# Kernel tuning notes

Measured on AMD Instinct MI355X. Metric: run time of the kernel, lower is better.

The kernel has to match this reference:

```python
import jax, jax.numpy as jnp
import numpy as np

DT = 0.1
B_SZ = 8192
T_HIST = 20
LEN_PRED = 30
FEAT = 32
N_LAYERS = 3
# state transition for constant-acceleration model (matches self.F in torch)
F_MAT = np.array([[1.0, DT, DT * DT / 2], [0.0, 1.0, DT], [0.0, 0.0, 1.0]], dtype=np.float32)


def setup_inputs() -> dict:
    key = jax.random.key(0)
    ks = jax.random.split(key, 16)
    # random-walk trajectories as history observations
    hist = jnp.cumsum(jax.random.normal(ks[0], (B_SZ, T_HIST, 2), jnp.float32) * 0.5, axis=1)
    k_lin = 1.0 / np.sqrt(FEAT)
    k_in = 1.0 / np.sqrt(24)

    def u(k, shape, scale):
        return jax.random.uniform(k, shape, jnp.float32, -scale, scale)

    return {
        "hist": hist,
        "max_accel_x": jnp.ones((1,), jnp.float32) * 10.0,
        "max_accel_y": jnp.ones((1,), jnp.float32) * 20.0,
        "velocity_std_x": jnp.ones((1,), jnp.float32) * 10.0,
        "acceleration_std_x": jnp.ones((1,), jnp.float32) * 10.0,
        "R_x_": jnp.array([0.0448], jnp.float32),
        "R_y_": jnp.array([0.001], jnp.float32),
        "G_x": jnp.array([0.0059, 0.2981, 0.0393], jnp.float32),
        "G_y": jnp.array([0.0059, 0.2981, 0.0393], jnp.float32) / 5.0,
        "Win_W": u(ks[1], (FEAT, 24), k_in),
        "Win_b": u(ks[2], (FEAT,), k_in),
        "enc_Wih": u(ks[3], (N_LAYERS, 4 * FEAT, FEAT), k_lin),
        "enc_Whh": u(ks[4], (N_LAYERS, 4 * FEAT, FEAT), k_lin),
        "enc_bih": u(ks[5], (N_LAYERS, 4 * FEAT), k_lin),
        "enc_bhh": u(ks[6], (N_LAYERS, 4 * FEAT), k_lin),
        "dec_Wih": u(ks[7], (N_LAYERS, 4 * FEAT, FEAT), k_lin),
        "dec_Whh": u(ks[8], (N_LAYERS, 4 * FEAT, FEAT), k_lin),
        "dec_bih": u(ks[9], (N_LAYERS, 4 * FEAT), k_lin),
        "dec_bhh": u(ks[10], (N_LAYERS, 4 * FEAT), k_lin),
        "Wout_W": u(ks[11], (4, FEAT), k_lin),
        "Wout_b": u(ks[12], (4,), k_lin),
        "len_pred": LEN_PRED,
    }


def reference(hist, max_accel_x, max_accel_y, velocity_std_x, acceleration_std_x,
              R_x_, R_y_, G_x, G_y, Win_W, Win_b,
              enc_Wih, enc_Whh, enc_bih, enc_bhh,
              dec_Wih, dec_Whh, dec_bih, dec_bhh,
              Wout_W, Wout_b, len_pred):
    B = hist.shape[0]
    F = jnp.asarray(F_MAT)
    R_x = R_x_[0] * R_x_[0]
    R_y = R_y_[0] * R_y_[0]
    Z_x = hist[:, :, 0]
    Z_y = hist[:, :, 1]

    def lstm(x, h, c, Wih, Whh, bih, bhh):
        g = x @ Wih.T + bih + h @ Whh.T + bhh
        i, f, gg, o = jnp.split(g, 4, axis=1)
        c = jax.nn.sigmoid(f) * c + jax.nn.sigmoid(i) * jnp.tanh(gg)
        h = jax.nn.sigmoid(o) * jnp.tanh(c)
        return h, c

    def stack(XP, h, c, Wih, Whh, bih, bhh):
        x = jnp.tanh(XP @ Win_W.T + Win_b)
        hs, cs = [], []
        for j in range(N_LAYERS):
            hj, cj = lstm(x, h[j], c[j], Wih[j], Whh[j], bih[j], bhh[j])
            hs.append(hj)
            cs.append(cj)
            x = cj  # torch code feeds the fresh CELL state to the next layer
        return jnp.stack(hs), jnp.stack(cs)

    def kpred(X, P, Q):
        return X @ F.T, jnp.einsum('ij,bjk,lk->bil', F, P, F) + Q

    def kupdate(X, P, z, R):
        y = z - X[:, 0]                      # innovation (H picks component 0)
        S = P[:, 0, 0] + R                   # innovation covariance (scalar)
        K = P[:, :, 0] / S[:, None]          # Kalman gain (B,3)
        return X + y[:, None] * K, P - K[:, :, None] * P[:, 0:1, :]

    def kinit(z0):
        # torch always calls _kalman_init with is_x=True (default), so both
        # axes use R_x / velocity_std_x / acceleration_std_x
        X = jnp.zeros((B, 3), hist.dtype).at[:, 0].set(z0)
        d = jnp.stack([R_x, velocity_std_x[0] ** 2, acceleration_std_x[0] ** 2])
        P = jnp.zeros((B, 3, 3), hist.dtype).at[:, jnp.arange(3), jnp.arange(3)].set(d)
        return X, P

    Qx_e = jnp.outer(G_x * max_accel_x[0], G_x * max_accel_x[0])
    Qy_e = jnp.outer(G_y * max_accel_y[0], G_y * max_accel_y[0])

    Xx, Px = kinit(Z_x[:, 0])
    Xy, Py = kinit(Z_y[:, 0])
    h = jnp.zeros((N_LAYERS, B, FEAT), hist.dtype)
    c = jnp.zeros_like(h)

    def enc_step(carry, zs):
        Xx, Px, Xy, Py, h, c = carry
        zx, zy = zs
        XP = jnp.concatenate([Xx, Xy, Px.reshape(B, 9), Py.reshape(B, 9)], 1)
        h, c = stack(XP, h, c, enc_Wih, enc_Whh, enc_bih, enc_bhh)
        Xx, Px = kpred(Xx, Px, Qx_e)
        Xy, Py = kpred(Xy, Py, Qy_e)
        Xx, Px = kupdate(Xx, Px, zx, R_x)
        Xy, Py = kupdate(Xy, Py, zy, R_y)
        return (Xx, Px, Xy, Py, h, c), None

    carry, _ = jax.lax.scan(enc_step, (Xx, Px, Xy, Py, h, c),
                            (Z_x[:, 1:].T, Z_y[:, 1:].T))

    oxx = jnp.outer(G_x, G_x)
    oyy = jnp.outer(G_y, G_y)

    def dec_step(carry, _):
        Xx, Px, Xy, Py, h, c = carry
        XP = jnp.concatenate([Xx, Xy, Px.reshape(B, 9), Py.reshape(B, 9)], 1)
        h, c = stack(XP, h, c, dec_Wih, dec_Whh, dec_bih, dec_bhh)
        pred = c[-1] @ Wout_W.T + Wout_b  # (B,4): [u_x, u_y, std_x, std_y]
        Xx = Xx.at[:, 2].set(DT * pred[:, 0])  # X[:,2] = B*u
        Xy = Xy.at[:, 2].set(DT * pred[:, 1])
        Qx = (pred[:, 2] ** 2)[:, None, None] * oxx
        Qy = (pred[:, 3] ** 2)[:, None, None] * oyy
        Xx, Px = kpred(Xx, Px, Qx)
        Xy, Py = kpred(Xy, Py, Qy)
        out = jnp.stack([Xx[:, 0], Xy[:, 0],
                         jnp.sqrt(Px[:, 0, 0]), jnp.sqrt(Py[:, 0, 0]),
                         jnp.zeros(B, hist.dtype)], axis=1)  # (B,5)
        return (Xx, Px, Xy, Py, h, c), out

    carry, ys = jax.lax.scan(dec_step, carry, None, length=len_pred)
    return jnp.transpose(ys, (1, 0, 2))  # (B, len_pred, 5)
```

## Files before the change

kernel.cpp:

```cpp
#include <hip/hip_runtime.h>
#include <math.h>

#define DT   0.1f
#define HDT  0.005f
#define T_HIST 20
#define LEN_PRED 30

typedef __attribute__((ext_vector_type(8))) short bfrag8;
typedef __attribute__((ext_vector_type(4))) short short4v;
typedef __attribute__((ext_vector_type(4))) float f32x4;

#define WS_FRAG   0u
#define WS_WIN    98304u
#define WS_WOUT   100352u
#define WS_BIAS   101376u

static __device__ __forceinline__ unsigned short f2bf(float x) {
    union { float f; unsigned int u; } v; v.f = x;
    unsigned int r = v.u + 0x7fffu + ((v.u >> 16) & 1u);
    return (unsigned short)(r >> 16);
}

__global__ void prep_kernel(const float* __restrict__ Win_W,
                            const float* __restrict__ eWih, const float* __restrict__ eWhh,
                            const float* __restrict__ ebih, const float* __restrict__ ebhh,
                            const float* __restrict__ dWih, const float* __restrict__ dWhh,
                            const float* __restrict__ dbih, const float* __restrict__ dbhh,
                            const float* __restrict__ Wout_W,
                            char* __restrict__ ws)
{
    int i = blockIdx.x * blockDim.x + threadIdx.x;
    if (i < 49152) {
        int fi = i >> 9, within = i & 511;
        int lane = within >> 3, jj = within & 7;
        int c = fi & 1, j = (fi >> 1) & 1, wvv = (fi >> 2) & 3;
        int pl = fi >> 4;
        int l = pl % 3, ph = pl / 3;
        int m = lane & 15, q2 = lane >> 4;
        int gate = m & 3;
        int feat = wvv * 8 + 4 * j + (m >> 2);
        int row = gate * 32 + feat;
        int k = q2 * 8 + jj;
        const float* W = (c == 0) ? (ph ? dWih : eWih) : (ph ? dWhh : eWhh);
        ((unsigned short*)(ws + WS_FRAG))[i] = f2bf(W[l * 4096 + row * 32 + k]);
    } else if (i < 50176) {
        int i2 = i - 49152;
        int w = i2 >> 9, within = i2 & 511;
        int lane = within >> 3, jj = within & 7;
        int m = lane & 15, q2 = lane >> 4;
        int k = q2 * 8 + jj;
        float v = (k < 24) ? Win_W[(w * 16 + m) * 24 + k] : 0.f;
        ((unsigned short*)(ws + WS_WIN))[i2] = f2bf(v);
    } else if (i < 50688) {
        int i3 = i - 50176;
        int lane = i3 >> 3, jj = i3 & 7;
        int m = lane & 15, q2 = lane >> 4;
        float v = (m < 4) ? Wout_W[m * 32 + q2 * 8 + jj] : 0.f;
        ((unsigned short*)(ws + WS_WOUT))[i3] = f2bf(v);
    } else if (i < 51456) {
        int b = i - 50688;
        int ph = b / 384, rem = b % 384;
        int l = rem >> 7, row = rem & 127;
        const float* bi = ph ? dbih : ebih;
        const float* bh = ph ? dbhh : ebhh;
        ((float*)(ws + WS_BIAS))[b] = bi[l * 128 + row] + bh[l * 128 + row];
    }
}

__launch_bounds__(256, 2)
__global__ void kalman_lstm_kernel(const float* __restrict__ hist,
                                   const float* __restrict__ max_ax, const float* __restrict__ max_ay,
                                   const float* __restrict__ vstd, const float* __restrict__ astd,
                                   const float* __restrict__ Rx_, const float* __restrict__ Ry_,
                                   const float* __restrict__ Gx, const float* __restrict__ Gy,
                                   const float* __restrict__ Win_b, const float* __restrict__ Wout_b,
                                   const char* __restrict__ ws, float* __restrict__ out)
{
    __shared__ __align__(16) unsigned short xin[4][16][40];
    __shared__ __align__(16) unsigned short hbuf[2][3][16][40];
    __shared__ __align__(16) unsigned short xpw[2][16][40];

    const int tid  = threadIdx.x;
    const int wv   = tid >> 6;
    const int lane = tid & 63;
    const int q    = lane >> 4;
    const int m    = lane & 15;
    const int b_elem = blockIdx.x * 16 + m;

    bfrag8 fragA[3][2][2];
    float  biasR[3][2][4];
    const bfrag8* fragp = (const bfrag8*)(ws + WS_FRAG);
    const float*  combp = (const float*)(ws + WS_BIAS);
    auto load_phase = [&](int ph) {
#pragma unroll
        for (int l = 0; l < 3; ++l)
#pragma unroll
            for (int j = 0; j < 2; ++j) {
#pragma unroll
                for (int c = 0; c < 2; ++c) {
                    int fi = (((ph * 3 + l) * 4 + wv) * 2 + j) * 2 + c;
                    fragA[l][j][c] = fragp[fi * 64 + lane];
                }
#pragma unroll
                for (int r = 0; r < 4; ++r)
                    biasR[l][j][r] = combp[ph * 384 + l * 128 + r * 32 + (wv * 8 + 4 * j + q)];
            }
    };
    load_phase(0);

    bfrag8 winF = {}, woutF = {};
    f32x4 winB = {0.f, 0.f, 0.f, 0.f};
    float wb0 = 0.f, wb1 = 0.f, wb2 = 0.f, wb3 = 0.f;
    float g0 = 0.f, g1 = 0.f, g2 = 0.f, ge0 = 0.f, ge1 = 0.f, ge2 = 0.f;
    float Rch = 0.f, X0 = 0.f, X1 = 0.f, X2 = 0.f;
    float P00 = 0.f, P01 = 0.f, P02 = 0.f, P11 = 0.f, P12 = 0.f, P22 = 0.f;
    const int ch = q & 1;
    if (wv >= 2) {
        int w = wv - 2;
        winF  = ((const bfrag8*)(ws + WS_WIN))[w * 64 + lane];
        woutF = ((const bfrag8*)(ws + WS_WOUT))[lane];
#pragma unroll
        for (int r = 0; r < 4; ++r) winB[r] = Win_b[w * 16 + q * 4 + r];
        wb0 = Wout_b[0]; wb1 = Wout_b[1]; wb2 = Wout_b[2]; wb3 = Wout_b[3];
        const float rx = Rx_[0] * Rx_[0], ry = Ry_[0] * Ry_[0];
        Rch = ch ? ry : rx;
        if (ch == 0) { g0 = Gx[0]; g1 = Gx[1]; g2 = Gx[2]; float s = max_ax[0]; ge0 = g0*s; ge1 = g1*s; ge2 = g2*s; }
        else         { g0 = Gy[0]; g1 = Gy[1]; g2 = Gy[2]; float s = max_ay[0]; ge0 = g0*s; ge1 = g1*s; ge2 = g2*s; }
        X0 = hist[b_elem * (T_HIST * 2) + ch];
        P00 = Rch; P11 = vstd[0] * vstd[0]; P22 = astd[0] * astd[0];
    }

    float creg[3][2];
#pragma unroll
    for (int l = 0; l < 3; ++l) { creg[l][0] = 0.f; creg[l][1] = 0.f; }

    for (int idx = tid; idx < 4 * 16 * 40; idx += 256) (&xin[0][0][0])[idx] = 0;
    for (int idx = tid; idx < 2 * 3 * 16 * 40; idx += 256) (&hbuf[0][0][0][0])[idx] = 0;
    for (int idx = tid; idx < 2 * 16 * 40; idx += 256) (&xpw[0][0][0])[idx] = 0;

    auto sig = [](float z) { return __builtin_amdgcn_rcpf(1.f + __expf(-z)); };
    auto th  = [](float z) { return fmaf(-2.f, __builtin_amdgcn_rcpf(__expf(2.f * z) + 1.f), 1.f); };

    auto kpred = [&](float Q00, float Q01, float Q02, float Q11, float Q12, float Q22) {
        X0 = X0 + DT * X1 + HDT * X2;
        X1 = X1 + DT * X2;
        float M00 = P00 + DT * P01 + HDT * P02;
        float M01 = P01 + DT * P11 + HDT * P12;
        float M02 = P02 + DT * P12 + HDT * P22;
        float M11 = P11 + DT * P12;
        float M12 = P12 + DT * P22;
        float M22 = P22;
        P00 = M00 + DT * M01 + HDT * M02 + Q00;
        P01 = M01 + DT * M02 + Q01;
        P02 = M02 + Q02;
        P11 = M11 + DT * M12 + Q11;
        P12 = M12 + Q12;
        P22 = M22 + Q22;
    };
    auto kupdate = [&](float z) {
        float y = z - X0;
        float Sinv = 1.0f / (P00 + Rch);
        float K0 = P00 * Sinv, K1 = P01 * Sinv, K2 = P02 * Sinv;
        X0 += y * K0; X1 += y * K1; X2 += y * K2;
        float p00 = P00, p01 = P01, p02 = P02;
        P00 = p00 - K0 * p00;
        P01 = p01 - K0 * p01;
        P02 = p02 - K0 * p02;
        P11 = P11 - K1 * p01;
        P12 = P12 - K1 * p02;
        P22 = P22 - K2 * p02;
    };
    auto write_xp = [&]() {
        if (q < 2) {
            unsigned short* row = &xpw[wv - 2][m][0];
            int o = ch * 3;
            row[o + 0] = f2bf(X0); row[o + 1] = f2bf(X1); row[o + 2] = f2bf(X2);
            int pb = 6 + ch * 9;
            row[pb + 0] = f2bf(P00); row[pb + 1] = f2bf(P01); row[pb + 2] = f2bf(P02);
            row[pb + 3] = f2bf(P01); row[pb + 4] = f2bf(P11); row[pb + 5] = f2bf(P12);
            row[pb + 6] = f2bf(P02); row[pb + 7] = f2bf(P12); row[pb + 8] = f2bf(P22);
        }
    };

    const f32x4 zero4 = {0.f, 0.f, 0.f, 0.f};

    auto regionA = [&](int mode, int t) {
        if (wv >= 2) {
            if (mode == 0) {
                if (t > 0) {
                    float z = hist[b_elem * (T_HIST * 2) + t * 2 + ch];
                    kpred(ge0 * ge0, ge0 * ge1, ge0 * ge2, ge1 * ge1, ge1 * ge2, ge2 * ge2);
                    kupdate(z);
                }
            } else {
                if (t == 0) {
                    float z = hist[b_elem * (T_HIST * 2) + 19 * 2 + ch];
                    kpred(ge0 * ge0, ge0 * ge1, ge0 * ge2, ge1 * ge1, ge1 * ge2, ge2 * ge2);
                    kupdate(z);
                } else {
                    bfrag8 bc2 = *(const bfrag8*)&xin[3][m][q * 8];
                    f32x4 ap = __builtin_amdgcn_mfma_f32_16x16x32_bf16(woutF, bc2, zero4, 0, 0, 0);
                    float a0 = ap[0] + wb0, a1 = ap[1] + wb1, a2 = ap[2] + wb2, a3 = ap[3] + wb3;
                    float s0 = __shfl(a0, m), s1 = __shfl(a1, m);
                    float s2 = __shfl(a2, m), s3 = __shfl(a3, m);
                    float pe = ch ? s1 : s0;
                    float qe = ch ? s3 : s2;
                    X2 = DT * pe;
                    float qs = qe * qe;
                    kpred(qs*g0*g0, qs*g0*g1, qs*g0*g2, qs*g1*g1, qs*g1*g2, qs*g2*g2);
                    if (wv == 2 && q < 2) {
                        float* o = out + (size_t)b_elem * (LEN_PRED * 5) + (t - 1) * 5;
                        if (ch == 0) { o[0] = X0; o[2] = sqrtf(P00); }
                        else         { o[1] = X0; o[3] = sqrtf(P00); o[4] = 0.f; }
                    }
                }
            }
            write_xp();
            bfrag8 bxp = *(const bfrag8*)&xpw[wv - 2][m][q * 8];
            f32x4 aw = __builtin_amdgcn_mfma_f32_16x16x32_bf16(winF, bxp, zero4, 0, 0, 0);
            union { short4v v; unsigned short s[4]; } u;
#pragma unroll
            for (int r = 0; r < 4; ++r) u.s[r] = f2bf(th(aw[r] + winB[r]));
            *(short4v*)&xin[0][m][(wv - 2) * 16 + q * 4] = u.v;
        }
        __syncthreads();
    };

    auto layers = [&](int p) {
#pragma unroll
        for (int l = 0; l < 3; ++l) {
            bfrag8 bx = *(const bfrag8*)&xin[l][m][q * 8];
            bfrag8 bh = *(const bfrag8*)&hbuf[p][l][m][q * 8];
            f32x4 a0 = __builtin_amdgcn_mfma_f32_16x16x32_bf16(fragA[l][0][0], bx, zero4, 0, 0, 0);
            a0        = __builtin_amdgcn_mfma_f32_16x16x32_bf16(fragA[l][0][1], bh, a0, 0, 0, 0);
            f32x4 a1 = __builtin_amdgcn_mfma_f32_16x16x32_bf16(fragA[l][1][0], bx, zero4, 0, 0, 0);
            a1        = __builtin_amdgcn_mfma_f32_16x16x32_bf16(fragA[l][1][1], bh, a1, 0, 0, 0);
#pragma unroll
            for (int j = 0; j < 2; ++j) {
                f32x4 a = j ? a1 : a0;
                float iv = sig(a[0] + biasR[l][j][0]);
                float fv = sig(a[1] + biasR[l][j][1]);
                float gv = th (a[2] + biasR[l][j][2]);
                float ov = sig(a[3] + biasR[l][j][3]);
                float cn = fmaf(fv, creg[l][j], iv * gv);
                float hn = ov * th(cn);
                creg[l][j] = cn;
                int f = wv * 8 + 4 * j + q;
                xin[l + 1][m][f] = f2bf(cn);
                hbuf[p ^ 1][l][m][f] = f2bf(hn);
            }
            __syncthreads();
        }
    };

    __syncthreads();
    int p = 0;

    for (int t = 0; t < T_HIST - 1; ++t) { regionA(0, t); layers(p); p ^= 1; }
    load_phase(1);
    for (int t = 0; t < LEN_PRED; ++t)   { regionA(1, t); layers(p); p ^= 1; }

    if (wv == 2) {
        bfrag8 bc2 = *(const bfrag8*)&xin[3][m][q * 8];
        f32x4 ap = __builtin_amdgcn_mfma_f32_16x16x32_bf16(woutF, bc2, zero4, 0, 0, 0);
        float a0 = ap[0] + wb0, a1 = ap[1] + wb1, a2 = ap[2] + wb2, a3 = ap[3] + wb3;
        float s0 = __shfl(a0, m), s1 = __shfl(a1, m);
        float s2 = __shfl(a2, m), s3 = __shfl(a3, m);
        float pe = ch ? s1 : s0;
        float qe = ch ? s3 : s2;
        X2 = DT * pe;
        float qs = qe * qe;
        kpred(qs*g0*g0, qs*g0*g1, qs*g0*g2, qs*g1*g1, qs*g1*g2, qs*g2*g2);
        if (q < 2) {
            float* o = out + (size_t)b_elem * (LEN_PRED * 5) + (LEN_PRED - 1) * 5;
            if (ch == 0) { o[0] = X0; o[2] = sqrtf(P00); }
            else         { o[1] = X0; o[3] = sqrtf(P00); o[4] = 0.f; }
        }
    }
}

extern "C" void kernel_launch(void* const* d_in, const int* in_sizes, int n_in,
                              void* d_out, int out_size, void* d_ws, size_t ws_size,
                              hipStream_t stream)
{
    const float* hist  = (const float*)d_in[0];
    const float* maxax = (const float*)d_in[1];
    const float* maxay = (const float*)d_in[2];
    const float* vstd  = (const float*)d_in[3];
    const float* astd  = (const float*)d_in[4];
    const float* Rx    = (const float*)d_in[5];
    const float* Ry    = (const float*)d_in[6];
    const float* Gx    = (const float*)d_in[7];
    const float* Gy    = (const float*)d_in[8];
    const float* WinW  = (const float*)d_in[9];
    const float* Winb  = (const float*)d_in[10];
    const float* eWih  = (const float*)d_in[11];
    const float* eWhh  = (const float*)d_in[12];
    const float* ebih  = (const float*)d_in[13];
    const float* ebhh  = (const float*)d_in[14];
    const float* dWih  = (const float*)d_in[15];
    const float* dWhh  = (const float*)d_in[16];
    const float* dbih  = (const float*)d_in[17];
    const float* dbhh  = (const float*)d_in[18];
    const float* WoutW = (const float*)d_in[19];
    const float* Woutb = (const float*)d_in[20];
    char* ws = (char*)d_ws;
    float* out = (float*)d_out;

    prep_kernel<<<202, 256, 0, stream>>>(WinW, eWih, eWhh, ebih, ebhh,
                                         dWih, dWhh, dbih, dbhh, WoutW, ws);
    kalman_lstm_kernel<<<512, 256, 0, stream>>>(hist, maxax, maxay, vstd, astd,
                                                Rx, Ry, Gx, Gy, Winb, Woutb,
                                                ws, out);
}
```

Measured before the change: 193.9 us.

## Split LSTM gate MFMA and activation across 8 waves, fold exp scaling into weights

The block grows from 256 to 512 threads. Waves 0-3 run the gate MFMAs and write the pre-activations to LDS, all 8 waves then apply the activations with one feature per lane, and waves 6-7 run the Kalman/input projection. The sigmoid and tanh scaling constants (-log2e, 2log2e) are folded into the weights and biases at prep time, so activations reduce to exp2 plus rcp. Biases are moved from registers into the MFMA accumulator init, loaded from LDS. This spreads the serial transcendental work across more lanes, at the cost of an extra LDS round trip and an extra barrier per layer.

After: 260.7 us. 34.5% more time.

```diff
diff --git a/kernel.cpp b/kernel.cpp
--- a/kernel.cpp
+++ b/kernel.cpp
@@ -5,6 +5,8 @@
 #define HDT  0.005f
 #define T_HIST 20
 #define LEN_PRED 30
+#define NLOG2E   (-1.4426950408889634f)
+#define TWOLOG2E ( 2.8853900817779268f)
 
 typedef __attribute__((ext_vector_type(8))) short bfrag8;
 typedef __attribute__((ext_vector_type(4))) short short4v;
@@ -19,6 +21,10 @@
     union { float f; unsigned int u; } v; v.f = x;
     unsigned int r = v.u + 0x7fffu + ((v.u >> 16) & 1u);
     return (unsigned short)(r >> 16);
+}
+
+static __device__ __forceinline__ float rcp1(float z) {
+    return __builtin_amdgcn_rcpf(1.f + __builtin_amdgcn_exp2f(z));
 }
 
 __global__ void prep_kernel(const float* __restrict__ Win_W,
@@ -41,15 +47,16 @@
         int feat = wvv * 8 + 4 * j + (m >> 2);
         int row = gate * 32 + feat;
         int k = q2 * 8 + jj;
+        float scale = (gate == 2) ? TWOLOG2E : NLOG2E;
         const float* W = (c == 0) ? (ph ? dWih : eWih) : (ph ? dWhh : eWhh);
-        ((unsigned short*)(ws + WS_FRAG))[i] = f2bf(W[l * 4096 + row * 32 + k]);
+        ((unsigned short*)(ws + WS_FRAG))[i] = f2bf(W[l * 4096 + row * 32 + k] * scale);
     } else if (i < 50176) {
         int i2 = i - 49152;
         int w = i2 >> 9, within = i2 & 511;
         int lane = within >> 3, jj = within & 7;
         int m = lane & 15, q2 = lane >> 4;
         int k = q2 * 8 + jj;
-        float v = (k < 24) ? Win_W[(w * 16 + m) * 24 + k] : 0.f;
+        float v = (k < 24) ? Win_W[(w * 16 + m) * 24 + k] * TWOLOG2E : 0.f;
         ((unsigned short*)(ws + WS_WIN))[i2] = f2bf(v);
     } else if (i < 50688) {
         int i3 = i - 50176;
@@ -60,14 +67,17 @@
     } else if (i < 51456) {
         int b = i - 50688;
         int ph = b / 384, rem = b % 384;
-        int l = rem >> 7, row = rem & 127;
+        int l = rem >> 7, fg = rem & 127;
+        int feat = fg >> 2, gate = fg & 3;
+        int row = gate * 32 + feat;
+        float scale = (gate == 2) ? TWOLOG2E : NLOG2E;
         const float* bi = ph ? dbih : ebih;
         const float* bh = ph ? dbhh : ebhh;
-        ((float*)(ws + WS_BIAS))[b] = bi[l * 128 + row] + bh[l * 128 + row];
+        ((float*)(ws + WS_BIAS))[b] = (bi[l * 128 + row] + bh[l * 128 + row]) * scale;
     }
 }
 
-__launch_bounds__(256, 2)
+__launch_bounds__(512, 2)
 __global__ void kalman_lstm_kernel(const float* __restrict__ hist,
                                    const float* __restrict__ max_ax, const float* __restrict__ max_ay,
                                    const float* __restrict__ vstd, const float* __restrict__ astd,
@@ -79,6 +89,8 @@
     __shared__ __align__(16) unsigned short xin[4][16][40];
     __shared__ __align__(16) unsigned short hbuf[2][3][16][40];
     __shared__ __align__(16) unsigned short xpw[2][16][40];
+    __shared__ __align__(16) float bias_lds[2][3][32][4];
+    __shared__ __align__(16) float pre[512][4];
 
     const int tid  = threadIdx.x;
     const int wv   = tid >> 6;
@@ -88,25 +100,19 @@
     const int b_elem = blockIdx.x * 16 + m;
 
     bfrag8 fragA[3][2][2];
-    float  biasR[3][2][4];
     const bfrag8* fragp = (const bfrag8*)(ws + WS_FRAG);
-    const float*  combp = (const float*)(ws + WS_BIAS);
     auto load_phase = [&](int ph) {
 #pragma unroll
         for (int l = 0; l < 3; ++l)
 #pragma unroll
-            for (int j = 0; j < 2; ++j) {
+            for (int j = 0; j < 2; ++j)
 #pragma unroll
                 for (int c = 0; c < 2; ++c) {
                     int fi = (((ph * 3 + l) * 4 + wv) * 2 + j) * 2 + c;
                     fragA[l][j][c] = fragp[fi * 64 + lane];
                 }
-#pragma unroll
-                for (int r = 0; r < 4; ++r)
-                    biasR[l][j][r] = combp[ph * 384 + l * 128 + r * 32 + (wv * 8 + 4 * j + q)];
-            }
-    };
-    load_phase(0);
+    };
+    if (wv < 4) load_phase(0);
 
     bfrag8 winF = {}, woutF = {};
     f32x4 winB = {0.f, 0.f, 0.f, 0.f};
@@ -115,12 +121,12 @@
     float Rch = 0.f, X0 = 0.f, X1 = 0.f, X2 = 0.f;
     float P00 = 0.f, P01 = 0.f, P02 = 0.f, P11 = 0.f, P12 = 0.f, P22 = 0.f;
     const int ch = q & 1;
-    if (wv >= 2) {
-        int w = wv - 2;
+    if (wv >= 6) {
+        int w = wv - 6;
         winF  = ((const bfrag8*)(ws + WS_WIN))[w * 64 + lane];
         woutF = ((const bfrag8*)(ws + WS_WOUT))[lane];
 #pragma unroll
-        for (int r = 0; r < 4; ++r) winB[r] = Win_b[w * 16 + q * 4 + r];
+        for (int r = 0; r < 4; ++r) winB[r] = Win_b[w * 16 + q * 4 + r] * TWOLOG2E;
         wb0 = Wout_b[0]; wb1 = Wout_b[1]; wb2 = Wout_b[2]; wb3 = Wout_b[3];
         const float rx = Rx_[0] * Rx_[0], ry = Ry_[0] * Ry_[0];
         Rch = ch ? ry : rx;
@@ -130,16 +136,13 @@
         P00 = Rch; P11 = vstd[0] * vstd[0]; P22 = astd[0] * astd[0];
     }
 
-    float creg[3][2];
-#pragma unroll
-    for (int l = 0; l < 3; ++l) { creg[l][0] = 0.f; creg[l][1] = 0.f; }
-
-    for (int idx = tid; idx < 4 * 16 * 40; idx += 256) (&xin[0][0][0])[idx] = 0;
-    for (int idx = tid; idx < 2 * 3 * 16 * 40; idx += 256) (&hbuf[0][0][0][0])[idx] = 0;
-    for (int idx = tid; idx < 2 * 16 * 40; idx += 256) (&xpw[0][0][0])[idx] = 0;
-
-    auto sig = [](float z) { return __builtin_amdgcn_rcpf(1.f + __expf(-z)); };
-    auto th  = [](float z) { return fmaf(-2.f, __builtin_amdgcn_rcpf(__expf(2.f * z) + 1.f), 1.f); };
+    float creg[3] = {0.f, 0.f, 0.f};
+
+    for (int idx = tid; idx < 768; idx += 512)
+        ((float*)bias_lds)[idx] = ((const float*)(ws + WS_BIAS))[idx];
+    for (int idx = tid; idx < 4 * 16 * 40; idx += 512) (&xin[0][0][0])[idx] = 0;
+    for (int idx = tid; idx < 2 * 3 * 16 * 40; idx += 512) (&hbuf[0][0][0][0])[idx] = 0;
+    for (int idx = tid; idx < 2 * 16 * 40; idx += 512) (&xpw[0][0][0])[idx] = 0;
 
     auto kpred = [&](float Q00, float Q01, float Q02, float Q11, float Q12, float Q22) {
         X0 = X0 + DT * X1 + HDT * X2;
@@ -170,9 +173,9 @@
         P12 = P12 - K1 * p02;
         P22 = P22 - K2 * p02;
     };
-    auto write_xp = [&]() {
+    auto write_xp = [&](int w) {
         if (q < 2) {
-            unsigned short* row = &xpw[wv - 2][m][0];
+            unsigned short* row = &xpw[w][m][0];
             int o = ch * 3;
             row[o + 0] = f2bf(X0); row[o + 1] = f2bf(X1); row[o + 2] = f2bf(X2);
             int pb = 6 + ch * 9;
@@ -185,7 +188,8 @@
     const f32x4 zero4 = {0.f, 0.f, 0.f, 0.f};
 
     auto regionA = [&](int mode, int t) {
-        if (wv >= 2) {
+        if (wv >= 6) {
+            int w = wv - 6;
             if (mode == 0) {
                 if (t > 0) {
                     float z = hist[b_elem * (T_HIST * 2) + t * 2 + ch];
@@ -208,59 +212,64 @@
                     X2 = DT * pe;
                     float qs = qe * qe;
                     kpred(qs*g0*g0, qs*g0*g1, qs*g0*g2, qs*g1*g1, qs*g1*g2, qs*g2*g2);
-                    if (wv == 2 && q < 2) {
+                    if (wv == 6 && q < 2) {
                         float* o = out + (size_t)b_elem * (LEN_PRED * 5) + (t - 1) * 5;
                         if (ch == 0) { o[0] = X0; o[2] = sqrtf(P00); }
                         else         { o[1] = X0; o[3] = sqrtf(P00); o[4] = 0.f; }
                     }
                 }
             }
-            write_xp();
-            bfrag8 bxp = *(const bfrag8*)&xpw[wv - 2][m][q * 8];
-            f32x4 aw = __builtin_amdgcn_mfma_f32_16x16x32_bf16(winF, bxp, zero4, 0, 0, 0);
+            write_xp(w);
+            bfrag8 bxp = *(const bfrag8*)&xpw[w][m][q * 8];
+            f32x4 aw = __builtin_amdgcn_mfma_f32_16x16x32_bf16(winF, bxp, winB, 0, 0, 0);
             union { short4v v; unsigned short s[4]; } u;
 #pragma unroll
-            for (int r = 0; r < 4; ++r) u.s[r] = f2bf(th(aw[r] + winB[r]));
-            *(short4v*)&xin[0][m][(wv - 2) * 16 + q * 4] = u.v;
+            for (int r = 0; r < 4; ++r) u.s[r] = f2bf(fmaf(-2.f, rcp1(aw[r]), 1.f));
+            *(short4v*)&xin[0][m][w * 16 + q * 4] = u.v;
         }
         __syncthreads();
     };
 
-    auto layers = [&](int p) {
+    auto layers = [&](int ph, int p) {
 #pragma unroll
         for (int l = 0; l < 3; ++l) {
-            bfrag8 bx = *(const bfrag8*)&xin[l][m][q * 8];
-            bfrag8 bh = *(const bfrag8*)&hbuf[p][l][m][q * 8];
-            f32x4 a0 = __builtin_amdgcn_mfma_f32_16x16x32_bf16(fragA[l][0][0], bx, zero4, 0, 0, 0);
-            a0        = __builtin_amdgcn_mfma_f32_16x16x32_bf16(fragA[l][0][1], bh, a0, 0, 0, 0);
-            f32x4 a1 = __builtin_amdgcn_mfma_f32_16x16x32_bf16(fragA[l][1][0], bx, zero4, 0, 0, 0);
-            a1        = __builtin_amdgcn_mfma_f32_16x16x32_bf16(fragA[l][1][1], bh, a1, 0, 0, 0);
-#pragma unroll
-            for (int j = 0; j < 2; ++j) {
-                f32x4 a = j ? a1 : a0;
-                float iv = sig(a[0] + biasR[l][j][0]);
-                float fv = sig(a[1] + biasR[l][j][1]);
-                float gv = th (a[2] + biasR[l][j][2]);
-                float ov = sig(a[3] + biasR[l][j][3]);
-                float cn = fmaf(fv, creg[l][j], iv * gv);
-                float hn = ov * th(cn);
-                creg[l][j] = cn;
-                int f = wv * 8 + 4 * j + q;
-                xin[l + 1][m][f] = f2bf(cn);
-                hbuf[p ^ 1][l][m][f] = f2bf(hn);
+            if (wv < 4) {
+                bfrag8 bx = *(const bfrag8*)&xin[l][m][q * 8];
+                bfrag8 bh = *(const bfrag8*)&hbuf[p][l][m][q * 8];
+                f32x4 b0 = *(const f32x4*)&bias_lds[ph][l][wv * 8 + q][0];
+                f32x4 b1 = *(const f32x4*)&bias_lds[ph][l][wv * 8 + 4 + q][0];
+                f32x4 t0 = __builtin_amdgcn_mfma_f32_16x16x32_bf16(fragA[l][0][0], bx, b0, 0, 0, 0);
+                f32x4 a0 = __builtin_amdgcn_mfma_f32_16x16x32_bf16(fragA[l][0][1], bh, t0, 0, 0, 0);
+                f32x4 t1 = __builtin_amdgcn_mfma_f32_16x16x32_bf16(fragA[l][1][0], bx, b1, 0, 0, 0);
+                f32x4 a1 = __builtin_amdgcn_mfma_f32_16x16x32_bf16(fragA[l][1][1], bh, t1, 0, 0, 0);
+                *(f32x4*)&pre[(wv * 8 + q) * 16 + m][0] = a0;
+                *(f32x4*)&pre[(wv * 8 + 4 + q) * 16 + m][0] = a1;
             }
             __syncthreads();
+            f32x4 g = *(const f32x4*)&pre[wv * 64 + lane][0];
+            float iv = rcp1(g[0]);
+            float fv = rcp1(g[1]);
+            float gv = fmaf(-2.f, rcp1(g[2]), 1.f);
+            float ov = rcp1(g[3]);
+            float cn = fmaf(fv, creg[l], iv * gv);
+            float tc = fmaf(-2.f, rcp1(cn * TWOLOG2E), 1.f);
+            float hn = ov * tc;
+            creg[l] = cn;
+            int f = (wv << 2) + q;
+            xin[l + 1][m][f] = f2bf(cn);
+            hbuf[p ^ 1][l][m][f] = f2bf(hn);
+            __syncthreads();
         }
     };
 
     __syncthreads();
     int p = 0;
 
-    for (int t = 0; t < T_HIST - 1; ++t) { regionA(0, t); layers(p); p ^= 1; }
-    load_phase(1);
-    for (int t = 0; t < LEN_PRED; ++t)   { regionA(1, t); layers(p); p ^= 1; }
-
-    if (wv == 2) {
+    for (int t = 0; t < T_HIST - 1; ++t) { regionA(0, t); layers(0, p); p ^= 1; }
+    if (wv < 4) load_phase(1);
+    for (int t = 0; t < LEN_PRED; ++t)   { regionA(1, t); layers(1, p); p ^= 1; }
+
+    if (wv == 6) {
         bfrag8 bc2 = *(const bfrag8*)&xin[3][m][q * 8];
         f32x4 ap = __builtin_amdgcn_mfma_f32_16x16x32_bf16(woutF, bc2, zero4, 0, 0, 0);
         float a0 = ap[0] + wb0, a1 = ap[1] + wb1, a2 = ap[2] + wb2, a3 = ap[3] + wb3;
@@ -309,7 +318,7 @@
 
     prep_kernel<<<202, 256, 0, stream>>>(WinW, eWih, eWhh, ebih, ebhh,
                                          dWih, dWhh, dbih, dbhh, WoutW, ws);
-    kalman_lstm_kernel<<<512, 256, 0, stream>>>(hist, maxax, maxay, vstd, astd,
+    kalman_lstm_kernel<<<512, 512, 0, stream>>>(hist, maxax, maxay, vstd, astd,
                                                 Rx, Ry, Gx, Gy, Winb, Woutb,
                                                 ws, out);
 }
```
